# Kernel optimization log

Measured on AMD Instinct MI355X. Metric: run time of the kernel, lower is better.

## Reference

```python
import jax, jax.numpy as jnp
import numpy as np

B, S, D = 8, 4096, 64
LN_EPS = 1e-3  # keras LayerNormalization default epsilon


def setup_inputs() -> dict:
    key = jax.random.key(0)
    k1, k2 = jax.random.split(key)
    x = jax.random.normal(k1, (B, S, D), dtype=jnp.float32)
    # (D,D,D) concept tensor, scaled small like glorot-ish init
    concept_map = jax.random.normal(k2, (D, D, D), dtype=jnp.float32) * 0.02
    gamma = jnp.ones((D,), dtype=jnp.float32)
    beta = jnp.zeros((D,), dtype=jnp.float32)
    return {"x": x, "concept_map": concept_map, "gamma": gamma, "beta": beta}


def reference(x, concept_map, gamma, beta):
    b, s, d = x.shape
    # Causal Toeplitz decay matrix: T[i, j] = 1/(i-j)^2 for j < i, else 0.
    idx = jnp.arange(s)
    diff = idx[:, None] - idx[None, :]  # (S, S)
    T = jnp.where(diff > 0, 1.0 / (jnp.maximum(diff, 1).astype(x.dtype) ** 2), 0.0)
    # Weighted causal prefix sum: S_pre[b, i, c] = sum_{j<i} x[b, j, c] / (i-j)^2
    s_pre = jnp.einsum('ij,bjc->bic', T, x)
    # Bilinear form with concept tensor: out[b,i,k] = sum_{a,c} x[b,i,a] * s_pre[b,i,c] * W[k,a,c]
    outer = (x[:, :, :, None] * s_pre[:, :, None, :]).reshape(b, s, d * d)  # (B,S,D*D)
    out = outer @ concept_map.reshape(d, d * d).T  # (B,S,D)
    # Residual + LayerNorm (axis=-1, keras defaults). Dropout is identity at inference.
    r = out + x
    mu = jnp.mean(r, axis=-1, keepdims=True)
    var = jnp.mean((r - mu) ** 2, axis=-1, keepdims=True)
    y = (r - mu) / jnp.sqrt(var + LN_EPS) * gamma + beta
    return y
```

## Files before the change

kernel.cpp:

```cpp
#include <hip/hip_runtime.h>

#define S_DIM 4096
#define B_DIM 8
#define D_DIM 64
#define LN_EPS 1e-3f

typedef _Float16 half8 __attribute__((ext_vector_type(8)));
typedef float f32x4 __attribute__((ext_vector_type(4)));

__device__ __forceinline__ void async_copy16(void* lds, const void* gsrc) {
    __builtin_amdgcn_global_load_lds(
        (const __attribute__((address_space(1))) unsigned int*)gsrc,
        (__attribute__((address_space(3))) unsigned int*)lds, 16, 0, 0);
}

__global__ __launch_bounds__(256) void prep_wt(const float* __restrict__ W,
                                               _Float16* __restrict__ wt) {
    int idx = blockIdx.x * 256 + threadIdx.x;
    int a = idx >> 12;
    int k = (idx >> 6) & 63;
    int c = idx & 63;
    wt[idx] = (_Float16)W[((k << 6) + a) * 64 + c];
}

__global__ __launch_bounds__(256) void stage1(const float* __restrict__ x,
                                              _Float16* __restrict__ s_out) {
    const int it = blockIdx.x;
    const int by = blockIdx.y;
    const int i0 = it * 64;
    const int tid = threadIdx.x;
    const int w = tid >> 6, l = tid & 63, lg = l >> 4, lr = l & 15;

    __shared__ _Float16 Bs[64 * 72];

    f32x4 acc[4] = {};
    const float iRowF = (float)(i0 + w * 16 + lr);
    const int ldC = tid & 63;
    const int ldJ = (tid >> 6) * 16;

    const int jt0 = (it >= 2) ? (it - 2) : 0;
    for (int jt = jt0; jt <= it; ++jt) {
        const int j0 = jt * 64;
        __syncthreads();
        {
            const float* xp = x + ((size_t)by * S_DIM + j0 + ldJ) * D_DIM + ldC;
            half8 v0, v1;
            #pragma unroll
            for (int q = 0; q < 8; ++q) {
                v0[q] = (_Float16)xp[q * D_DIM];
                v1[q] = (_Float16)xp[(8 + q) * D_DIM];
            }
            *(half8*)&Bs[ldC * 72 + ldJ] = v0;
            *(half8*)&Bs[ldC * 72 + ldJ + 8] = v1;
        }
        __syncthreads();
        #pragma unroll
        for (int kk = 0; kk < 2; ++kk) {
            half8 af;
            #pragma unroll
            for (int bq = 0; bq < 8; ++bq) {
                int j = j0 + kk * 32 + lg * 8 + bq;
                float df = iRowF - (float)j;
                float tv = (df > 0.f) ? __builtin_amdgcn_rcpf(df * df) : 0.f;
                af[bq] = (_Float16)tv;
            }
            #pragma unroll
            for (int nt = 0; nt < 4; ++nt) {
                half8 bf = *(const half8*)&Bs[(nt * 16 + lr) * 72 + kk * 32 + lg * 8];
                acc[nt] = __builtin_amdgcn_mfma_f32_16x16x32_f16(af, bf, acc[nt], 0, 0, 0);
            }
        }
    }

    #pragma unroll
    for (int nt = 0; nt < 4; ++nt) {
        #pragma unroll
        for (int r = 0; r < 4; ++r) {
            int i = i0 + w * 16 + lg * 4 + r;
            int c = nt * 16 + lr;
            s_out[((size_t)by * S_DIM + i) * D_DIM + c] = (_Float16)acc[nt][r];
        }
    }
}

__global__ __launch_bounds__(512, 4) void stage2(const float* __restrict__ x,
                                                 const _Float16* __restrict__ s,
                                                 const _Float16* __restrict__ wt,
                                                 const float* __restrict__ gamma,
                                                 const float* __restrict__ beta,
                                                 float* __restrict__ out) {
    const int r0 = blockIdx.x * 64;
    const int tid = threadIdx.x;
    const int w = tid >> 6, l = tid & 63, lg = l >> 4, lr = l & 15;
    const int rg = w & 1;
    const int ah = w >> 1;

    __shared__ __align__(16) char smem[9216 + 2 * 32768];
    _Float16* Xf = (_Float16*)smem;
    char* WbB = smem + 9216;
    float* P = (float*)(smem + 9216);

    const int laneSrc = ((l >> 3) * 128) + ((((l & 7) ^ (l >> 3)) << 4));
    const char* wbase = (const char*)wt;

#define STAGE(t, buf)                                                          \
    {                                                                          \
        _Pragma("unroll")                                                      \
        for (int i_ = 0; i_ < 4; ++i_) {                                       \
            int c_ = w * 4 + i_;                                               \
            int q_ = c_ >> 3, sub_ = c_ & 7;                                   \
            const char* g_ = wbase + (size_t)(q_ * 16 + (t)) * 8192            \
                             + sub_ * 1024 + laneSrc;                          \
            char* l_ = WbB + (buf) * 32768 + q_ * 8192 + sub_ * 1024;          \
            async_copy16(l_, g_);                                              \
        }                                                                      \
    }

    STAGE(0, 0);

    {
        int row = tid >> 3, c0 = (tid & 7) * 8;
        const float* xp = x + (size_t)(r0 + row) * 64 + c0;
        half8 v;
        #pragma unroll
        for (int j = 0; j < 8; ++j) v[j] = (_Float16)xp[j];
        *(half8*)&Xf[row * 72 + c0] = v;
    }

    half8 sf[2][2];
    #pragma unroll
    for (int rt = 0; rt < 2; ++rt) {
        size_t row = (size_t)(r0 + rg * 32 + rt * 16 + lr) * 64;
        sf[rt][0] = *(const half8*)&s[row + lg * 8];
        sf[rt][1] = *(const half8*)&s[row + 32 + lg * 8];
    }

    __syncthreads();

    half8 xav[2][2];
    #pragma unroll
    for (int rt = 0; rt < 2; ++rt)
        #pragma unroll
        for (int q = 0; q < 2; ++q) {
            int ro = (rg * 32 + rt * 16 + lr) * 72 + ah * 16 + q * 8;
            xav[rt][q] = *(const half8*)&Xf[ro];
        }

    f32x4 acc[2][4] = {};
    const int swz0 = (lg * 16) ^ ((lr & 7) << 4);
    const int swz1 = (64 + lg * 16) ^ ((lr & 7) << 4);

    #pragma unroll
    for (int t = 0; t < 16; ++t) {
        const int buf = t & 1;
        if (t + 1 < 16) STAGE(t + 1, buf ^ 1);
        const char* wa = WbB + buf * 32768 + ah * 8192;
        _Float16 xa0 = xav[0][t >> 3][t & 7];
        _Float16 xa1 = xav[1][t >> 3][t & 7];
        half8 af00 = sf[0][0] * xa0, af01 = sf[0][1] * xa0;
        half8 af10 = sf[1][0] * xa1, af11 = sf[1][1] * xa1;
        #pragma unroll
        for (int nt = 0; nt < 4; ++nt) {
            const char* rp = wa + (nt * 16 + lr) * 128;
            half8 b0 = *(const half8*)(rp + swz0);
            half8 b1 = *(const half8*)(rp + swz1);
            acc[0][nt] = __builtin_amdgcn_mfma_f32_16x16x32_f16(af00, b0, acc[0][nt], 0, 0, 0);
            acc[0][nt] = __builtin_amdgcn_mfma_f32_16x16x32_f16(af01, b1, acc[0][nt], 0, 0, 0);
            acc[1][nt] = __builtin_amdgcn_mfma_f32_16x16x32_f16(af10, b0, acc[1][nt], 0, 0, 0);
            acc[1][nt] = __builtin_amdgcn_mfma_f32_16x16x32_f16(af11, b1, acc[1][nt], 0, 0, 0);
        }
        __syncthreads();
    }

    if (ah != 0) {
        const int ph = ah - 1;
        #pragma unroll
        for (int rt = 0; rt < 2; ++rt)
            #pragma unroll
            for (int nt = 0; nt < 4; ++nt)
                #pragma unroll
                for (int reg = 0; reg < 4; ++reg) {
                    int row_l = rg * 32 + rt * 16 + lg * 4 + reg;
                    P[ph * 4224 + row_l * 66 + nt * 16 + lr] = acc[rt][nt][reg];
                }
    }
    __syncthreads();

    if (ah == 0) {
        float gba[4], bta[4];
        #pragma unroll
        for (int nt = 0; nt < 4; ++nt) {
            gba[nt] = gamma[nt * 16 + lr];
            bta[nt] = beta[nt * 16 + lr];
        }
        #pragma unroll
        for (int rt = 0; rt < 2; ++rt) {
            float rv[4][4], sum[4], ssq[4];
            #pragma unroll
            for (int reg = 0; reg < 4; ++reg) {
                int row_l = rg * 32 + rt * 16 + lg * 4 + reg;
                size_t gr = (size_t)(r0 + row_l);
                float s_ = 0.f, q_ = 0.f;
                #pragma unroll
                for (int nt = 0; nt < 4; ++nt) {
                    int col = nt * 16 + lr;
                    float v = acc[rt][nt][reg]
                            + P[row_l * 66 + col]
                            + P[4224 + row_l * 66 + col]
                            + P[8448 + row_l * 66 + col]
                            + x[gr * 64 + col];
                    rv[nt][reg] = v;
                    s_ += v;
                    q_ += v * v;
                }
                sum[reg] = s_;
                ssq[reg] = q_;
            }
            #pragma unroll
            for (int m = 1; m < 16; m <<= 1) {
                #pragma unroll
                for (int reg = 0; reg < 4; ++reg) {
                    sum[reg] += __shfl_xor(sum[reg], m, 64);
                    ssq[reg] += __shfl_xor(ssq[reg], m, 64);
                }
            }
            #pragma unroll
            for (int reg = 0; reg < 4; ++reg) {
                float mean = sum[reg] * (1.f / 64.f);
                float var = ssq[reg] * (1.f / 64.f) - mean * mean;
                float rstd = __frsqrt_rn(var + LN_EPS);
                int gr = r0 + rg * 32 + rt * 16 + lg * 4 + reg;
                #pragma unroll
                for (int nt = 0; nt < 4; ++nt) {
                    float y = (rv[nt][reg] - mean) * rstd * gba[nt] + bta[nt];
                    out[(size_t)gr * 64 + nt * 16 + lr] = y;
                }
            }
        }
    }
#undef STAGE
}

extern "C" void kernel_launch(void* const* d_in, const int* in_sizes, int n_in,
                              void* d_out, int out_size, void* d_ws, size_t ws_size,
                              hipStream_t stream) {
    const float* x     = (const float*)d_in[0];
    const float* W     = (const float*)d_in[1];
    const float* gamma = (const float*)d_in[2];
    const float* beta  = (const float*)d_in[3];
    float* outp        = (float*)d_out;

    char* ws = (char*)d_ws;
    _Float16* s_f16 = (_Float16*)ws;
    _Float16* wt    = (_Float16*)(ws + (size_t)B_DIM * S_DIM * D_DIM * 2);

    prep_wt<<<(64 * 64 * 64) / 256, 256, 0, stream>>>(W, wt);
    stage1<<<dim3(S_DIM / 64, B_DIM), 256, 0, stream>>>(x, s_f16);
    stage2<<<(B_DIM * S_DIM) / 64, 512, 0, stream>>>(x, s_f16, wt, gamma, beta, outp);
}
```

Measured before the change: 36.41 us.

## Merge prep and stage1 kernels; double stage2 row tile and deepen W prefetch

Merges the weight-transpose kernel and the causal-prefix kernel into one launch, with blocks split by index, to save a launch and its drain. Stage2 now processes 128 rows per block instead of 64, so each staged W tile feeds twice as many MFMAs and the weight traffic per row is halved. The W pipeline prefetches two tiles ahead with explicit vmcnt waits and raw barriers in place of __syncthreads. The cost is more registers, larger LDS use and lower occupancy (launch bounds go from 4 to 2 blocks), plus only 256 stage2 blocks to spread across the CUs.

```diff
diff --git a/kernel.cpp b/kernel.cpp
--- a/kernel.cpp
+++ b/kernel.cpp
@@ -14,19 +14,21 @@
         (__attribute__((address_space(3))) unsigned int*)lds, 16, 0, 0);
 }
 
-__global__ __launch_bounds__(256) void prep_wt(const float* __restrict__ W,
-                                               _Float16* __restrict__ wt) {
-    int idx = blockIdx.x * 256 + threadIdx.x;
-    int a = idx >> 12;
-    int k = (idx >> 6) & 63;
-    int c = idx & 63;
-    wt[idx] = (_Float16)W[((k << 6) + a) * 64 + c];
-}
-
-__global__ __launch_bounds__(256) void stage1(const float* __restrict__ x,
-                                              _Float16* __restrict__ s_out) {
-    const int it = blockIdx.x;
-    const int by = blockIdx.y;
+__global__ __launch_bounds__(256) void prep_stage1(const float* __restrict__ x,
+                                                   const float* __restrict__ W,
+                                                   _Float16* __restrict__ wt,
+                                                   _Float16* __restrict__ s_out) {
+    if (blockIdx.x < 1024) {
+        int idx = blockIdx.x * 256 + threadIdx.x;
+        int a = idx >> 12;
+        int k = (idx >> 6) & 63;
+        int c = idx & 63;
+        wt[idx] = (_Float16)W[((k << 6) + a) * 64 + c];
+        return;
+    }
+    const int lin = blockIdx.x - 1024;
+    const int it = lin & 63;
+    const int by = lin >> 6;
     const int i0 = it * 64;
     const int tid = threadIdx.x;
     const int w = tid >> 6, l = tid & 63, lg = l >> 4, lr = l & 15;
@@ -83,22 +85,22 @@
     }
 }
 
-__global__ __launch_bounds__(512, 4) void stage2(const float* __restrict__ x,
+__global__ __launch_bounds__(512, 2) void stage2(const float* __restrict__ x,
                                                  const _Float16* __restrict__ s,
                                                  const _Float16* __restrict__ wt,
                                                  const float* __restrict__ gamma,
                                                  const float* __restrict__ beta,
                                                  float* __restrict__ out) {
-    const int r0 = blockIdx.x * 64;
+    const int r0 = blockIdx.x * 128;
     const int tid = threadIdx.x;
     const int w = tid >> 6, l = tid & 63, lg = l >> 4, lr = l & 15;
     const int rg = w & 1;
     const int ah = w >> 1;
 
-    __shared__ __align__(16) char smem[9216 + 2 * 32768];
+    __shared__ __align__(16) char smem[101376];
     _Float16* Xf = (_Float16*)smem;
-    char* WbB = smem + 9216;
-    float* P = (float*)(smem + 9216);
+    char* WbB = smem + 18432;
+    float* P = (float*)smem;
 
     const int laneSrc = ((l >> 3) * 128) + ((((l & 7) ^ (l >> 3)) << 4));
     const char* wbase = (const char*)wt;
@@ -117,71 +119,84 @@
     }
 
     STAGE(0, 0);
+    STAGE(1, 1);
 
     {
-        int row = tid >> 3, c0 = (tid & 7) * 8;
-        const float* xp = x + (size_t)(r0 + row) * 64 + c0;
-        half8 v;
-        #pragma unroll
-        for (int j = 0; j < 8; ++j) v[j] = (_Float16)xp[j];
-        *(half8*)&Xf[row * 72 + c0] = v;
-    }
-
-    half8 sf[2][2];
-    #pragma unroll
-    for (int rt = 0; rt < 2; ++rt) {
-        size_t row = (size_t)(r0 + rg * 32 + rt * 16 + lr) * 64;
+        #pragma unroll
+        for (int h = 0; h < 2; ++h) {
+            int idx = h * 512 + tid;
+            int row = idx >> 3, c0 = (idx & 7) * 8;
+            const float* xp = x + (size_t)(r0 + row) * 64 + c0;
+            half8 v;
+            #pragma unroll
+            for (int j = 0; j < 8; ++j) v[j] = (_Float16)xp[j];
+            *(half8*)&Xf[row * 72 + c0] = v;
+        }
+    }
+
+    half8 sf[4][2];
+    #pragma unroll
+    for (int rt = 0; rt < 4; ++rt) {
+        size_t row = (size_t)(r0 + rg * 64 + rt * 16 + lr) * 64;
         sf[rt][0] = *(const half8*)&s[row + lg * 8];
         sf[rt][1] = *(const half8*)&s[row + 32 + lg * 8];
     }
 
     __syncthreads();
 
-    half8 xav[2][2];
-    #pragma unroll
-    for (int rt = 0; rt < 2; ++rt)
-        #pragma unroll
-        for (int q = 0; q < 2; ++q) {
-            int ro = (rg * 32 + rt * 16 + lr) * 72 + ah * 16 + q * 8;
-            xav[rt][q] = *(const half8*)&Xf[ro];
-        }
-
-    f32x4 acc[2][4] = {};
+    half8 xav[4][2];
+    #pragma unroll
+    for (int rt = 0; rt < 4; ++rt)
+        #pragma unroll
+        for (int q = 0; q < 2; ++q)
+            xav[rt][q] = *(const half8*)&Xf[(rg * 64 + rt * 16 + lr) * 72 + ah * 16 + q * 8];
+
+    f32x4 acc[4][4] = {};
     const int swz0 = (lg * 16) ^ ((lr & 7) << 4);
     const int swz1 = (64 + lg * 16) ^ ((lr & 7) << 4);
 
     #pragma unroll
     for (int t = 0; t < 16; ++t) {
-        const int buf = t & 1;
-        if (t + 1 < 16) STAGE(t + 1, buf ^ 1);
-        const char* wa = WbB + buf * 32768 + ah * 8192;
-        _Float16 xa0 = xav[0][t >> 3][t & 7];
-        _Float16 xa1 = xav[1][t >> 3][t & 7];
-        half8 af00 = sf[0][0] * xa0, af01 = sf[0][1] * xa0;
-        half8 af10 = sf[1][0] * xa1, af11 = sf[1][1] * xa1;
+        const char* wa = WbB + (t & 1) * 32768 + ah * 8192;
+        half8 af[4][2];
+        #pragma unroll
+        for (int rt = 0; rt < 4; ++rt) {
+            _Float16 xa = xav[rt][t >> 3][t & 7];
+            af[rt][0] = sf[rt][0] * xa;
+            af[rt][1] = sf[rt][1] * xa;
+        }
         #pragma unroll
         for (int nt = 0; nt < 4; ++nt) {
             const char* rp = wa + (nt * 16 + lr) * 128;
             half8 b0 = *(const half8*)(rp + swz0);
             half8 b1 = *(const half8*)(rp + swz1);
-            acc[0][nt] = __builtin_amdgcn_mfma_f32_16x16x32_f16(af00, b0, acc[0][nt], 0, 0, 0);
-            acc[0][nt] = __builtin_amdgcn_mfma_f32_16x16x32_f16(af01, b1, acc[0][nt], 0, 0, 0);
-            acc[1][nt] = __builtin_amdgcn_mfma_f32_16x16x32_f16(af10, b0, acc[1][nt], 0, 0, 0);
-            acc[1][nt] = __builtin_amdgcn_mfma_f32_16x16x32_f16(af11, b1, acc[1][nt], 0, 0, 0);
-        }
-        __syncthreads();
+            #pragma unroll
+            for (int rt = 0; rt < 4; ++rt) {
+                acc[rt][nt] = __builtin_amdgcn_mfma_f32_16x16x32_f16(af[rt][0], b0, acc[rt][nt], 0, 0, 0);
+                acc[rt][nt] = __builtin_amdgcn_mfma_f32_16x16x32_f16(af[rt][1], b1, acc[rt][nt], 0, 0, 0);
+            }
+        }
+        __builtin_amdgcn_s_barrier();
+        if (t + 2 < 16) STAGE(t + 2, t & 1);
+        if (t < 14) {
+            asm volatile("s_waitcnt vmcnt(4)" ::: "memory");
+            __builtin_amdgcn_s_barrier();
+        } else if (t == 14) {
+            asm volatile("s_waitcnt vmcnt(0)" ::: "memory");
+            __builtin_amdgcn_s_barrier();
+        }
     }
 
     if (ah != 0) {
         const int ph = ah - 1;
         #pragma unroll
-        for (int rt = 0; rt < 2; ++rt)
+        for (int rt = 0; rt < 4; ++rt)
             #pragma unroll
             for (int nt = 0; nt < 4; ++nt)
                 #pragma unroll
                 for (int reg = 0; reg < 4; ++reg) {
-                    int row_l = rg * 32 + rt * 16 + lg * 4 + reg;
-                    P[ph * 4224 + row_l * 66 + nt * 16 + lr] = acc[rt][nt][reg];
+                    int row_l = rg * 64 + rt * 16 + lg * 4 + reg;
+                    P[ph * 8448 + row_l * 66 + nt * 16 + lr] = acc[rt][nt][reg];
                 }
     }
     __syncthreads();
@@ -194,11 +209,11 @@
             bta[nt] = beta[nt * 16 + lr];
         }
         #pragma unroll
-        for (int rt = 0; rt < 2; ++rt) {
+        for (int rt = 0; rt < 4; ++rt) {
             float rv[4][4], sum[4], ssq[4];
             #pragma unroll
             for (int reg = 0; reg < 4; ++reg) {
-                int row_l = rg * 32 + rt * 16 + lg * 4 + reg;
+                int row_l = rg * 64 + rt * 16 + lg * 4 + reg;
                 size_t gr = (size_t)(r0 + row_l);
                 float s_ = 0.f, q_ = 0.f;
                 #pragma unroll
@@ -206,8 +221,8 @@
                     int col = nt * 16 + lr;
                     float v = acc[rt][nt][reg]
                             + P[row_l * 66 + col]
-                            + P[4224 + row_l * 66 + col]
                             + P[8448 + row_l * 66 + col]
+                            + P[16896 + row_l * 66 + col]
                             + x[gr * 64 + col];
                     rv[nt][reg] = v;
                     s_ += v;
@@ -229,7 +244,7 @@
                 float mean = sum[reg] * (1.f / 64.f);
                 float var = ssq[reg] * (1.f / 64.f) - mean * mean;
                 float rstd = __frsqrt_rn(var + LN_EPS);
-                int gr = r0 + rg * 32 + rt * 16 + lg * 4 + reg;
+                int gr = r0 + rg * 64 + rt * 16 + lg * 4 + reg;
                 #pragma unroll
                 for (int nt = 0; nt < 4; ++nt) {
                     float y = (rv[nt][reg] - mean) * rstd * gba[nt] + bta[nt];
@@ -254,7 +269,6 @@
     _Float16* s_f16 = (_Float16*)ws;
     _Float16* wt    = (_Float16*)(ws + (size_t)B_DIM * S_DIM * D_DIM * 2);
 
-    prep_wt<<<(64 * 64 * 64) / 256, 256, 0, stream>>>(W, wt);
-    stage1<<<dim3(S_DIM / 64, B_DIM), 256, 0, stream>>>(x, s_f16);
-    stage2<<<(B_DIM * S_DIM) / 64, 512, 0, stream>>>(x, s_f16, wt, gamma, beta, outp);
-}
+    prep_stage1<<<1024 + 512, 256, 0, stream>>>(x, W, wt, s_f16);
+    stage2<<<(B_DIM * S_DIM) / 128, 512, 0, stream>>>(x, s_f16, wt, gamma, beta, outp);
+}
```

Result: faster. 33.71 us (-7.4%).
